# Performance work log

Measured on AMD Instinct MI355X. Metric: run time of the kernel, lower is better.

Reference implementation:

```python
import jax, jax.numpy as jnp
import numpy as np

B, N, NC, C = 8, 16384, 64, 256

def setup_inputs() -> dict:
    key = jax.random.key(0)
    k1, k2, k3, k4, k5, k6 = jax.random.split(key, 6)
    s = 1.0 / np.sqrt(C)
    return {
        "point_features": jax.random.normal(k1, (B, N, C), dtype=jnp.float32),
        "centroid_features": jax.random.normal(k2, (B, NC, C), dtype=jnp.float32),
        "W_p": jax.random.uniform(k3, (C, C), jnp.float32, -s, s),   # point_transform weight (in,out)
        "b_p": jax.random.uniform(k4, (C,), jnp.float32, -s, s),
        "W_c": jax.random.uniform(k5, (C, C), jnp.float32, -s, s),   # centroid_transform weight (in,out)
        "b_c": jax.random.uniform(k6, (C,), jnp.float32, -s, s),
    }

def reference(point_features, centroid_features, W_p, b_p, W_c, b_c):
    # Linear projections
    p_proj = jnp.einsum('bnc,cd->bnd', point_features, W_p) + b_p      # (B,N,C)
    c_proj = jnp.einsum('bkc,cd->bkd', centroid_features, W_c) + b_c   # (B,NC,C)
    # Unscaled cross-attention scores and softmax over centroids
    scores = jnp.einsum('bnd,bkd->bnk', p_proj, c_proj)                # (B,N,NC)
    weights = jax.nn.softmax(scores, axis=-1)
    # Weighted sum of RAW centroid features (values not projected)
    weighted = jnp.einsum('bnk,bkc->bnc', weights, centroid_features)  # (B,N,C)
    return point_features + weighted
```

## Files before the change

### kernel.cpp

```cpp
#include <hip/hip_runtime.h>

#define B_  8
#define N_  16384
#define NC_ 64
#define C_  256

typedef __attribute__((ext_vector_type(8))) short bf16x8;
typedef __attribute__((ext_vector_type(4))) float f32x4;

#define WS_BLOB_OFF 262144
#define WS_S0_OFF   (262144 + 8*98304)

__device__ __forceinline__ unsigned rne_bf16(float f) {
    unsigned u = __float_as_uint(f);
    return (u + 0x7fffu + ((u >> 16) & 1u)) >> 16;
}

__device__ __forceinline__ f32x4 mfma16(bf16x8 a, bf16x8 b, f32x4 c) {
    return __builtin_amdgcn_mfma_f32_16x16x32_bf16(a, b, c, 0, 0, 0);
}

__global__ __launch_bounds__(256) void k_transpose(const float* __restrict__ A,
                                                   float* __restrict__ At) {
    __shared__ float t[16][17];
    int bi = blockIdx.x >> 4, bj = blockIdx.x & 15;
    int tx = threadIdx.x & 15, ty = threadIdx.x >> 4;
    t[ty][tx] = A[(bi*16 + ty)*C_ + bj*16 + tx];
    __syncthreads();
    At[(bj*16 + ty)*C_ + bi*16 + tx] = t[tx][ty];
}

__global__ __launch_bounds__(256) void k_pre(const float* __restrict__ Cf,
        const float* __restrict__ Wc, const float* __restrict__ bc,
        const float* __restrict__ bp, const float* __restrict__ WpT,
        char* __restrict__ blob, float* __restrict__ s0g) {
    int b  = blockIdx.x >> 3;
    int kg = blockIdx.x & 7;
    int t  = threadIdx.x;
    __shared__ float cfL[8][256];
    __shared__ float vL[8][256];

    const float* cfb = Cf + ((size_t)b*NC_ + kg*8) * C_;
    #pragma unroll
    for (int kk = 0; kk < 8; ++kk) cfL[kk][t] = cfb[kk*C_ + t];
    __syncthreads();

    float acc[8];
    float bcv = bc[t];
    #pragma unroll
    for (int kk = 0; kk < 8; ++kk) acc[kk] = bcv;
    #pragma unroll 4
    for (int c = 0; c < C_; ++c) {
        float wv = Wc[c*C_ + t];
        #pragma unroll
        for (int kk = 0; kk < 8; ++kk) acc[kk] = fmaf(cfL[kk][c], wv, acc[kk]);
    }
    #pragma unroll
    for (int kk = 0; kk < 8; ++kk) vL[kk][t] = acc[kk];
    __syncthreads();

    if (t < 64) {
        #pragma unroll
        for (int kk = 0; kk < 8; ++kk) {
            float s = 0.f;
            #pragma unroll
            for (int j = 0; j < 4; ++j) { int d = t + j*64; s += bp[d]*vL[kk][d]; }
            #pragma unroll
            for (int m = 32; m >= 1; m >>= 1) s += __shfl_xor(s, m);
            if (t == 0) s0g[b*NC_ + kg*8 + kk] = s;
        }
    }

    float vt[8];
    #pragma unroll
    for (int kk = 0; kk < 8; ++kk) vt[kk] = 0.f;
    #pragma unroll 4
    for (int d = 0; d < C_; ++d) {
        float wv = WpT[d*C_ + t];
        #pragma unroll
        for (int kk = 0; kk < 8; ++kk) vt[kk] = fmaf(wv, vL[kk][d], vt[kk]);
    }

    char* vhiB = blob + (size_t)b*98304;
    char* vloB = vhiB + 32768;
    char* cftB = vhiB + 65536;
    #pragma unroll
    for (int kk = 0; kk < 8; ++kk) {
        int row = kg*8 + kk;
        unsigned hb = rne_bf16(vt[kk]);
        float hf = __uint_as_float(hb << 16);
        unsigned lb = rne_bf16(vt[kk] - hf);
        unsigned off = ((unsigned)(row*512 + t*2)) ^ ((unsigned)(row & 15) << 4);
        *(unsigned short*)(vhiB + off) = (unsigned short)hb;
        *(unsigned short*)(vloB + off) = (unsigned short)lb;
        unsigned offc = ((unsigned)(t*128 + row*2)) ^ ((unsigned)(t & 7) << 4);
        *(unsigned short*)(cftB + offc) = (unsigned short)rne_bf16(cfL[kk][t]);
    }
}

__global__ __launch_bounds__(512, 2) void k_main(const float* __restrict__ P,
        const char* __restrict__ blob, const float* __restrict__ s0g,
        float* __restrict__ out) {
    __shared__ __align__(16) char smem[114944];
    float* s0L   = (float*)(smem + 98304);
    char*  wbAll = smem + 98560;

    const int nb = N_ / 128;
    int b    = blockIdx.x / nb;
    int tile = blockIdx.x % nb;
    int row_blk = tile * 128;
    int tid = threadIdx.x;
    int w   = tid >> 6;
    int l   = tid & 63;
    int l15 = l & 15;
    int g   = l >> 4;

    {
        const f32x4* src = (const f32x4*)(blob + (size_t)b*98304);
        f32x4* dst = (f32x4*)smem;
        #pragma unroll 4
        for (int i = tid; i < 6144; i += 512) dst[i] = src[i];
        if (tid < 64) s0L[tid] = s0g[b*NC_ + tid];
    }
    __syncthreads();

    int prow = row_blk + w*16 + l15;
    const float* Prow = P + ((size_t)b*N_ + prow)*C_ + g*8;
    f32x4 pf[16];
    #pragma unroll
    for (int kk = 0; kk < 8; ++kk) {
        pf[2*kk]   = *(const f32x4*)(Prow + kk*32);
        pf[2*kk+1] = *(const f32x4*)(Prow + kk*32 + 4);
    }

    f32x4 sacc[4];
    #pragma unroll
    for (int mf = 0; mf < 4; ++mf) {
        #pragma unroll
        for (int r = 0; r < 4; ++r) sacc[mf][r] = s0L[mf*16 + g*4 + r];
    }

    #pragma unroll
    for (int kk = 0; kk < 8; ++kk) {
        bf16x8 phi, plo;
        #pragma unroll
        for (int h = 0; h < 2; ++h) {
            #pragma unroll
            for (int j = 0; j < 4; ++j) {
                float f  = pf[2*kk + h][j];
                unsigned hb = rne_bf16(f);
                float hf = __uint_as_float(hb << 16);
                unsigned lb = rne_bf16(f - hf);
                phi[h*4 + j] = (short)hb;
                plo[h*4 + j] = (short)lb;
            }
        }
        #pragma unroll
        for (int mf = 0; mf < 4; ++mf) {
            unsigned off = ((unsigned)((mf*16 + l15)*512 + kk*64 + g*16)) ^ ((unsigned)l15 << 4);
            bf16x8 vh = *(const bf16x8*)(smem + off);
            bf16x8 vl = *(const bf16x8*)(smem + 32768 + off);
            sacc[mf] = mfma16(vh, phi, sacc[mf]);
            sacc[mf] = mfma16(vh, plo, sacc[mf]);
            sacc[mf] = mfma16(vl, phi, sacc[mf]);
        }
    }

    float mx = -3.0e38f;
    #pragma unroll
    for (int mf = 0; mf < 4; ++mf)
        #pragma unroll
        for (int r = 0; r < 4; ++r) mx = fmaxf(mx, sacc[mf][r]);
    mx = fmaxf(mx, __shfl_xor(mx, 16));
    mx = fmaxf(mx, __shfl_xor(mx, 32));
    float sum = 0.f;
    float pv[4][4];
    #pragma unroll
    for (int mf = 0; mf < 4; ++mf)
        #pragma unroll
        for (int r = 0; r < 4; ++r) {
            float e = __expf(sacc[mf][r] - mx);
            pv[mf][r] = e; sum += e;
        }
    sum += __shfl_xor(sum, 16);
    sum += __shfl_xor(sum, 32);
    float inv = 1.0f / sum;

    char* wb = wbAll + w*2048;
    #pragma unroll
    for (int mf = 0; mf < 4; ++mf) {
        unsigned w01 = rne_bf16(pv[mf][0]*inv) | (rne_bf16(pv[mf][1]*inv) << 16);
        unsigned w23 = rne_bf16(pv[mf][2]*inv) | (rne_bf16(pv[mf][3]*inv) << 16);
        unsigned off = ((unsigned)(l15*128 + mf*32 + g*8)) ^ ((unsigned)(l15 & 7) << 4);
        uint2 v; v.x = w01; v.y = w23;
        *(uint2*)(wb + off) = v;
    }

    f32x4 zero = {0.f, 0.f, 0.f, 0.f};
    f32x4 oacc[16];
    #pragma unroll
    for (int nf = 0; nf < 16; ++nf) oacc[nf] = zero;
    #pragma unroll
    for (int kk2 = 0; kk2 < 2; ++kk2) {
        unsigned woff = ((unsigned)(l15*128 + kk2*64 + g*16)) ^ ((unsigned)(l15 & 7) << 4);
        bf16x8 wf = *(const bf16x8*)(wb + woff);
        #pragma unroll
        for (int nf = 0; nf < 16; ++nf) {
            unsigned coff = ((unsigned)((nf*16 + l15)*128 + kk2*64 + g*16)) ^ ((unsigned)(l15 & 7) << 4);
            bf16x8 cf = *(const bf16x8*)(smem + 65536 + coff);
            oacc[nf] = mfma16(wf, cf, oacc[nf]);
        }
    }

    size_t obase = ((size_t)b*N_ + row_blk + w*16 + g*4) * C_;
    #pragma unroll
    for (int nf = 0; nf < 16; ++nf) {
        #pragma unroll
        for (int r = 0; r < 4; ++r) {
            size_t idx = obase + (size_t)r*C_ + nf*16 + l15;
            out[idx] = P[idx] + oacc[nf][r];
        }
    }
}

extern "C" void kernel_launch(void* const* d_in, const int* in_sizes, int n_in,
                              void* d_out, int out_size, void* d_ws, size_t ws_size,
                              hipStream_t stream) {
    const float* P  = (const float*)d_in[0];
    const float* Cf = (const float*)d_in[1];
    const float* Wp = (const float*)d_in[2];
    const float* bp = (const float*)d_in[3];
    const float* Wc = (const float*)d_in[4];
    const float* bc = (const float*)d_in[5];
    float* out = (float*)d_out;

    float* WpT = (float*)d_ws;
    char*  blob = (char*)d_ws + WS_BLOB_OFF;
    float* s0   = (float*)((char*)d_ws + WS_S0_OFF);

    k_transpose<<<256, 256, 0, stream>>>(Wp, WpT);
    k_pre<<<64, 256, 0, stream>>>(Cf, Wc, bc, bp, WpT, blob, s0);
    k_main<<<B_*(N_/128), 512, 0, stream>>>(P, blob, s0, out);
}
```

Baseline: 314.1 us.

## Precompute fused Wp·Wcᵀ, drop V low-part MFMA, shrink LDS, vectorize epilogue

The preprocessing now forms the combined matrix Wp·Wcᵀ once, plus the bias cross terms, and then applies it to the centroid features. This replaces the transpose kernel and the two-stage projection. The main kernel drops the low-precision correction term of V, going from three MFMAs to two per fragment and halving the V tile in LDS. That frees enough shared memory to raise occupancy from 2 to 4 blocks per CU. The bias is read directly from global memory, the blob copy overlaps with the P loads, and the output MFMA operands are swapped so each lane can load and store P/out as float4. Dropping the V low part and rounding V only to bf16 lowers score precision, which may raise numerical error through the unscaled softmax.

After: 290.2 us. -7.6%, faster.

```diff
diff --git a/kernel.cpp b/kernel.cpp
--- a/kernel.cpp
+++ b/kernel.cpp
@@ -8,8 +8,12 @@
 typedef __attribute__((ext_vector_type(8))) short bf16x8;
 typedef __attribute__((ext_vector_type(4))) float f32x4;
 
-#define WS_BLOB_OFF 262144
-#define WS_S0_OFF   (262144 + 8*98304)
+#define WS_GT   0
+#define WS_BLOB 262144
+#define WS_S0   786432
+#define WS_WFB  788480
+#define WS_H    789504
+#define WS_BB   790528
 
 __device__ __forceinline__ unsigned rne_bf16(float f) {
     unsigned u = __float_as_uint(f);
@@ -20,90 +24,114 @@
     return __builtin_amdgcn_mfma_f32_16x16x32_bf16(a, b, c, 0, 0, 0);
 }
 
-__global__ __launch_bounds__(256) void k_transpose(const float* __restrict__ A,
-                                                   float* __restrict__ At) {
-    __shared__ float t[16][17];
-    int bi = blockIdx.x >> 4, bj = blockIdx.x & 15;
-    int tx = threadIdx.x & 15, ty = threadIdx.x >> 4;
-    t[ty][tx] = A[(bi*16 + ty)*C_ + bj*16 + tx];
-    __syncthreads();
-    At[(bj*16 + ty)*C_ + bi*16 + tx] = t[tx][ty];
-}
-
-__global__ __launch_bounds__(256) void k_pre(const float* __restrict__ Cf,
+__global__ __launch_bounds__(256) void k_p1(const float* __restrict__ Wp,
         const float* __restrict__ Wc, const float* __restrict__ bc,
-        const float* __restrict__ bp, const float* __restrict__ WpT,
-        char* __restrict__ blob, float* __restrict__ s0g) {
-    int b  = blockIdx.x >> 3;
-    int kg = blockIdx.x & 7;
-    int t  = threadIdx.x;
-    __shared__ float cfL[8][256];
-    __shared__ float vL[8][256];
-
-    const float* cfb = Cf + ((size_t)b*NC_ + kg*8) * C_;
-    #pragma unroll
-    for (int kk = 0; kk < 8; ++kk) cfL[kk][t] = cfb[kk*C_ + t];
-    __syncthreads();
+        const float* __restrict__ bp, float* __restrict__ ws) {
+    __shared__ float WpL[256];
+    __shared__ float bpL[256];
+    __shared__ float red[4];
+    int c = blockIdx.x, t = threadIdx.x;
+    WpL[t] = Wp[(size_t)c*C_ + t];
+    bpL[t] = bp[t];
+    float bcv = bc[t];
+    __syncthreads();
+
+    const float* wcr = Wc + (size_t)t*C_;
+    float acc = 0.f;
+    #pragma unroll 8
+    for (int d = 0; d < C_; d += 4) {
+        f32x4 wv = *(const f32x4*)(wcr + d);
+        f32x4 wp = *(const f32x4*)(WpL + d);
+        acc += wv[0]*wp[0] + wv[1]*wp[1] + wv[2]*wp[2] + wv[3]*wp[3];
+    }
+    ws[WS_GT/4 + c*C_ + t] = acc;
+
+    float hp = bcv * WpL[t];
+    #pragma unroll
+    for (int m = 32; m; m >>= 1) hp += __shfl_xor(hp, m);
+    if ((t & 63) == 0) red[t >> 6] = hp;
+    __syncthreads();
+    if (t == 0) ws[WS_H/4 + c] = red[0] + red[1] + red[2] + red[3];
+
+    if (c == 0) {
+        float aw = 0.f;
+        #pragma unroll 8
+        for (int d = 0; d < C_; d += 4) {
+            f32x4 wv = *(const f32x4*)(wcr + d);
+            f32x4 b4 = *(const f32x4*)(bpL + d);
+            aw += wv[0]*b4[0] + wv[1]*b4[1] + wv[2]*b4[2] + wv[3]*b4[3];
+        }
+        ws[WS_WFB/4 + t] = aw;
+        float pb = bcv * bpL[t];
+        #pragma unroll
+        for (int m = 32; m; m >>= 1) pb += __shfl_xor(pb, m);
+        __syncthreads();
+        if ((t & 63) == 0) red[t >> 6] = pb;
+        __syncthreads();
+        if (t == 0) ws[WS_BB/4] = red[0] + red[1] + red[2] + red[3];
+    }
+}
+
+__global__ __launch_bounds__(256) void k_p2(const float* __restrict__ Cf,
+        float* __restrict__ ws) {
+    __shared__ float CfL[8][256];
+    __shared__ float wfbL[256];
+    int b = blockIdx.x >> 3, kg = blockIdx.x & 7;
+    int t = threadIdx.x;
+    const float* cfb = Cf + ((size_t)b*NC_ + kg*8)*C_;
+    #pragma unroll
+    for (int kk = 0; kk < 8; ++kk) CfL[kk][t] = cfb[kk*C_ + t];
+    wfbL[t] = ws[WS_WFB/4 + t];
+    float hv = ws[WS_H/4 + t];
+    float bb = ws[WS_BB/4];
+    __syncthreads();
+
+    char* vhiB = (char*)ws + WS_BLOB + (size_t)b*65536;
+    char* cftB = vhiB + 32768;
+
+    #pragma unroll
+    for (int kk = 0; kk < 8; ++kk) {
+        unsigned offc = ((unsigned)(t*128 + (kg*8 + kk)*2)) ^ ((unsigned)(t & 7) << 4);
+        *(unsigned short*)(cftB + offc) = (unsigned short)rne_bf16(CfL[kk][t]);
+    }
 
     float acc[8];
-    float bcv = bc[t];
-    #pragma unroll
-    for (int kk = 0; kk < 8; ++kk) acc[kk] = bcv;
+    #pragma unroll
+    for (int kk = 0; kk < 8; ++kk) acc[kk] = hv;
+    const float* gtr = ws + WS_GT/4 + (size_t)t*C_;
     #pragma unroll 4
-    for (int c = 0; c < C_; ++c) {
-        float wv = Wc[c*C_ + t];
-        #pragma unroll
-        for (int kk = 0; kk < 8; ++kk) acc[kk] = fmaf(cfL[kk][c], wv, acc[kk]);
-    }
-    #pragma unroll
-    for (int kk = 0; kk < 8; ++kk) vL[kk][t] = acc[kk];
-    __syncthreads();
-
-    if (t < 64) {
+    for (int e = 0; e < C_; e += 4) {
+        f32x4 g4 = *(const f32x4*)(gtr + e);
         #pragma unroll
         for (int kk = 0; kk < 8; ++kk) {
-            float s = 0.f;
-            #pragma unroll
-            for (int j = 0; j < 4; ++j) { int d = t + j*64; s += bp[d]*vL[kk][d]; }
-            #pragma unroll
-            for (int m = 32; m >= 1; m >>= 1) s += __shfl_xor(s, m);
-            if (t == 0) s0g[b*NC_ + kg*8 + kk] = s;
-        }
-    }
-
-    float vt[8];
-    #pragma unroll
-    for (int kk = 0; kk < 8; ++kk) vt[kk] = 0.f;
-    #pragma unroll 4
-    for (int d = 0; d < C_; ++d) {
-        float wv = WpT[d*C_ + t];
-        #pragma unroll
-        for (int kk = 0; kk < 8; ++kk) vt[kk] = fmaf(wv, vL[kk][d], vt[kk]);
-    }
-
-    char* vhiB = blob + (size_t)b*98304;
-    char* vloB = vhiB + 32768;
-    char* cftB = vhiB + 65536;
+            f32x4 c4 = *(const f32x4*)(&CfL[kk][e]);
+            acc[kk] += g4[0]*c4[0] + g4[1]*c4[1] + g4[2]*c4[2] + g4[3]*c4[3];
+        }
+    }
     #pragma unroll
     for (int kk = 0; kk < 8; ++kk) {
         int row = kg*8 + kk;
-        unsigned hb = rne_bf16(vt[kk]);
-        float hf = __uint_as_float(hb << 16);
-        unsigned lb = rne_bf16(vt[kk] - hf);
         unsigned off = ((unsigned)(row*512 + t*2)) ^ ((unsigned)(row & 15) << 4);
-        *(unsigned short*)(vhiB + off) = (unsigned short)hb;
-        *(unsigned short*)(vloB + off) = (unsigned short)lb;
-        unsigned offc = ((unsigned)(t*128 + row*2)) ^ ((unsigned)(t & 7) << 4);
-        *(unsigned short*)(cftB + offc) = (unsigned short)rne_bf16(cfL[kk][t]);
-    }
-}
-
-__global__ __launch_bounds__(512, 2) void k_main(const float* __restrict__ P,
+        *(unsigned short*)(vhiB + off) = (unsigned short)rne_bf16(acc[kk]);
+    }
+
+    int w = t >> 6, l = t & 63;
+    #pragma unroll
+    for (int kk = 2*w; kk < 2*w + 2; ++kk) {
+        float s = 0.f;
+        #pragma unroll
+        for (int j = 0; j < 4; ++j) s += CfL[kk][l + 64*j] * wfbL[l + 64*j];
+        #pragma unroll
+        for (int m = 32; m; m >>= 1) s += __shfl_xor(s, m);
+        if (l == 0) ws[WS_S0/4 + b*NC_ + kg*8 + kk] = s + bb;
+    }
+}
+
+__global__ __launch_bounds__(512, 4) void k_main(const float* __restrict__ P,
         const char* __restrict__ blob, const float* __restrict__ s0g,
         float* __restrict__ out) {
-    __shared__ __align__(16) char smem[114944];
-    float* s0L   = (float*)(smem + 98304);
-    char*  wbAll = smem + 98560;
+    __shared__ __align__(16) char smem[81920];
+    char* wbAll = smem + 65536;
 
     const int nb = N_ / 128;
     int b    = blockIdx.x / nb;
@@ -115,15 +143,6 @@
     int l15 = l & 15;
     int g   = l >> 4;
 
-    {
-        const f32x4* src = (const f32x4*)(blob + (size_t)b*98304);
-        f32x4* dst = (f32x4*)smem;
-        #pragma unroll 4
-        for (int i = tid; i < 6144; i += 512) dst[i] = src[i];
-        if (tid < 64) s0L[tid] = s0g[b*NC_ + tid];
-    }
-    __syncthreads();
-
     int prow = row_blk + w*16 + l15;
     const float* Prow = P + ((size_t)b*N_ + prow)*C_ + g*8;
     f32x4 pf[16];
@@ -132,13 +151,18 @@
         pf[2*kk]   = *(const f32x4*)(Prow + kk*32);
         pf[2*kk+1] = *(const f32x4*)(Prow + kk*32 + 4);
     }
-
     f32x4 sacc[4];
     #pragma unroll
-    for (int mf = 0; mf < 4; ++mf) {
-        #pragma unroll
-        for (int r = 0; r < 4; ++r) sacc[mf][r] = s0L[mf*16 + g*4 + r];
-    }
+    for (int mf = 0; mf < 4; ++mf)
+        sacc[mf] = *(const f32x4*)(s0g + b*NC_ + mf*16 + g*4);
+
+    {
+        const f32x4* src = (const f32x4*)(blob + (size_t)b*65536);
+        f32x4* dst = (f32x4*)smem;
+        #pragma unroll
+        for (int i = 0; i < 8; ++i) dst[tid + i*512] = src[tid + i*512];
+    }
+    __syncthreads();
 
     #pragma unroll
     for (int kk = 0; kk < 8; ++kk) {
@@ -159,10 +183,8 @@
         for (int mf = 0; mf < 4; ++mf) {
             unsigned off = ((unsigned)((mf*16 + l15)*512 + kk*64 + g*16)) ^ ((unsigned)l15 << 4);
             bf16x8 vh = *(const bf16x8*)(smem + off);
-            bf16x8 vl = *(const bf16x8*)(smem + 32768 + off);
             sacc[mf] = mfma16(vh, phi, sacc[mf]);
             sacc[mf] = mfma16(vh, plo, sacc[mf]);
-            sacc[mf] = mfma16(vl, phi, sacc[mf]);
         }
     }
 
@@ -207,19 +229,19 @@
         #pragma unroll
         for (int nf = 0; nf < 16; ++nf) {
             unsigned coff = ((unsigned)((nf*16 + l15)*128 + kk2*64 + g*16)) ^ ((unsigned)(l15 & 7) << 4);
-            bf16x8 cf = *(const bf16x8*)(smem + 65536 + coff);
-            oacc[nf] = mfma16(wf, cf, oacc[nf]);
-        }
-    }
-
-    size_t obase = ((size_t)b*N_ + row_blk + w*16 + g*4) * C_;
+            bf16x8 cf = *(const bf16x8*)(smem + 32768 + coff);
+            oacc[nf] = mfma16(cf, wf, oacc[nf]);
+        }
+    }
+
+    size_t rowbase = ((size_t)b*N_ + row_blk + w*16 + l15) * C_;
     #pragma unroll
     for (int nf = 0; nf < 16; ++nf) {
-        #pragma unroll
-        for (int r = 0; r < 4; ++r) {
-            size_t idx = obase + (size_t)r*C_ + nf*16 + l15;
-            out[idx] = P[idx] + oacc[nf][r];
-        }
+        size_t idx = rowbase + nf*16 + g*4;
+        f32x4 pr = *(const f32x4*)(P + idx);
+        f32x4 o  = oacc[nf];
+        f32x4 res = {pr[0]+o[0], pr[1]+o[1], pr[2]+o[2], pr[3]+o[3]};
+        *(f32x4*)(out + idx) = res;
     }
 }
 
@@ -233,12 +255,10 @@
     const float* Wc = (const float*)d_in[4];
     const float* bc = (const float*)d_in[5];
     float* out = (float*)d_out;
-
-    float* WpT = (float*)d_ws;
-    char*  blob = (char*)d_ws + WS_BLOB_OFF;
-    float* s0   = (float*)((char*)d_ws + WS_S0_OFF);
-
-    k_transpose<<<256, 256, 0, stream>>>(Wp, WpT);
-    k_pre<<<64, 256, 0, stream>>>(Cf, Wc, bc, bp, WpT, blob, s0);
-    k_main<<<B_*(N_/128), 512, 0, stream>>>(P, blob, s0, out);
-}
+    float* ws  = (float*)d_ws;
+
+    k_p1<<<256, 256, 0, stream>>>(Wp, Wc, bc, bp, ws);
+    k_p2<<<64, 256, 0, stream>>>(Cf, ws);
+    k_main<<<B_*(N_/128), 512, 0, stream>>>(P, (const char*)d_ws + WS_BLOB,
+                                            ws + WS_S0/4, out);
+}
```
